# Kernel optimization log

Hardware: AMD Instinct MI355X
Metric: run time of the kernel (lower is better)

Reference implementation:

```python
import jax, jax.numpy as jnp
import numpy as np

D_MODEL = 2816
N_HEADS = 16
DH = 512
N_KV = 2
MAX_CTX = 8192
POS = 4095  # current decode position (0-indexed)
EPS = 1e-6
Q_DIM = N_HEADS * DH
KV_DIM = N_KV * DH
NEG_INF = -1e9


def setup_inputs() -> dict:
    key = jax.random.key(0)
    ks = jax.random.split(key, 8)
    x = jax.random.normal(ks[0], (1, 1, D_MODEL), jnp.float32)
    # Realistic RoPE angles at position POS (full head_dim rotation, half/half layout)
    inv_freq = 1.0 / (10000.0 ** (np.arange(0, DH, 2, dtype=np.float32) / DH))  # (DH/2,)
    ang = POS * inv_freq
    cos = jnp.asarray(np.concatenate([np.cos(ang), np.cos(ang)])[None, None, :], jnp.float32)  # (1,1,DH)
    sin = jnp.asarray(np.concatenate([np.sin(ang), np.sin(ang)])[None, None, :], jnp.float32)
    k_cache = jax.random.normal(ks[1], (1, N_KV, MAX_CTX, DH), jnp.float32) * 0.02
    v_cache = jax.random.normal(ks[2], (1, N_KV, MAX_CTX, DH), jnp.float32) * 0.02
    # causal decode mask: attend to [0, POS], -inf beyond
    pos_ids = jnp.arange(MAX_CTX)
    attn_mask = jnp.where(pos_ids <= POS, 0.0, NEG_INF).astype(jnp.float32).reshape(1, 1, 1, MAX_CTX)
    # one-hot write mask at current position
    kv_write_mask = jnp.zeros((1, 1, MAX_CTX, 1), jnp.float32).at[0, 0, POS, 0].set(1.0)
    Wq = jax.random.normal(ks[3], (Q_DIM, D_MODEL), jnp.float32) * 0.02
    Wk = jax.random.normal(ks[4], (KV_DIM, D_MODEL), jnp.float32) * 0.02
    Wo = jax.random.normal(ks[5], (D_MODEL, Q_DIM), jnp.float32) * 0.02
    q_gamma = jax.random.normal(ks[6], (DH,), jnp.float32) * 0.02  # stored as (gamma-1)
    k_gamma = jax.random.normal(ks[7], (DH,), jnp.float32) * 0.02
    return {"x": x, "cos": cos, "sin": sin, "k_cache": k_cache, "v_cache": v_cache,
            "attn_mask": attn_mask, "kv_write_mask": kv_write_mask,
            "Wq": Wq, "Wk": Wk, "Wo": Wo, "q_gamma": q_gamma, "k_gamma": k_gamma}


def _rmsnorm(x, w=None):
    v = jnp.mean(x * x, axis=-1, keepdims=True)
    x = x * jax.lax.rsqrt(v + EPS)
    return x if w is None else x * (1.0 + w)


def _rope(x, cos, sin):
    # x: (1,T,H,D); cos/sin: (1,T,D)
    c = cos[:, :, None, :]
    s = sin[:, :, None, :]
    d = x.shape[-1]
    x1, x2 = x[..., : d // 2], x[..., d // 2 :]
    rot = jnp.concatenate([-x2, x1], axis=-1)
    return x * c + rot * s


def reference(x, cos, sin, k_cache, v_cache, attn_mask, kv_write_mask, Wq, Wk, Wo, q_gamma, k_gamma):
    q_raw = (x @ Wq.T).reshape(1, 1, N_HEADS, DH)
    k_raw = (x @ Wk.T).reshape(1, 1, N_KV, DH)
    q = _rope(_rmsnorm(q_raw, q_gamma), cos, sin)
    k = _rope(_rmsnorm(k_raw, k_gamma), cos, sin)
    v = _rmsnorm(k_raw)  # unscaled norm, not rotated
    q = jnp.swapaxes(q, 1, 2)  # (1,H,1,D)
    k = jnp.swapaxes(k, 1, 2)  # (1,n_kv,1,D)
    v = jnp.swapaxes(v, 1, 2)
    k_new = k_cache + k * kv_write_mask  # broadcast write at current slot
    v_new = v_cache + v * kv_write_mask
    rep = N_HEADS // N_KV
    K = jnp.repeat(k_new, rep, axis=1)  # (1,H,S,D)
    V = jnp.repeat(v_new, rep, axis=1)
    scores = jnp.einsum("bhtd,bhsd->bhts", q, K) + attn_mask  # no 1/sqrt(d) scale, as in source
    w = jax.nn.softmax(scores.astype(jnp.float32), axis=-1).astype(q.dtype)
    ctx = jnp.einsum("bhts,bhsd->bhtd", w, V)  # (1,H,1,D)
    ctx = jnp.swapaxes(ctx, 1, 2).reshape(1, 1, Q_DIM)
    out = ctx @ Wo.T
    return (out, k_new, v_new)
```

## Files before the change

### kernel.cpp

```cpp
#include <hip/hip_runtime.h>
#include <math.h>

#define D_MODEL 2816
#define N_HEADS 16
#define DH      512
#define N_KV    2
#define MAX_CTX 8192
#define POS     4095
#define EPS     1e-6f
#define Q_DIM   8192
#define KV_DIM  1024
#define GROUP   8
#define NPOS    4096
#define AB      128


__device__ __forceinline__ float4 f4_mul(float4 a, float s) {
  return make_float4(a.x*s, a.y*s, a.z*s, a.w*s);
}
__device__ __forceinline__ float4 f4_mul4(float4 a, float4 b) {
  return make_float4(a.x*b.x, a.y*b.y, a.z*b.z, a.w*b.w);
}
__device__ __forceinline__ float4 f4_fma(float4 a, float4 b, float4 c) {
  return make_float4(fmaf(a.x,b.x,c.x), fmaf(a.y,b.y,c.y), fmaf(a.z,b.z,c.z), fmaf(a.w,b.w,c.w));
}
__device__ __forceinline__ float4 f4_fmas(float s, float4 b, float4 c) {
  return make_float4(fmaf(s,b.x,c.x), fmaf(s,b.y,c.y), fmaf(s,b.z,c.z), fmaf(s,b.w,c.w));
}
__device__ __forceinline__ float4 f4_fnma(float4 a, float4 b, float4 c) {
  return make_float4(fmaf(-a.x,b.x,c.x), fmaf(-a.y,b.y,c.y), fmaf(-a.z,b.z,c.z), fmaf(-a.w,b.w,c.w));
}
__device__ __forceinline__ float4 f4_add(float4 a, float4 b) {
  return make_float4(a.x+b.x, a.y+b.y, a.z+b.z, a.w+b.w);
}
__device__ __forceinline__ float f4_dot(float4 a, float4 b) {
  return a.x*b.x + a.y*b.y + a.z*b.z + a.w*b.w;
}
__device__ __forceinline__ float f4_ssq(float4 a) {
  return a.x*a.x + a.y*a.y + a.z*a.z + a.w*a.w;
}

__global__ __launch_bounds__(256) void k_qkv(const float* __restrict__ x,
    const float* __restrict__ Wq, const float* __restrict__ Wk,
    float* __restrict__ qraw, float* __restrict__ kraw,
    float* __restrict__ ctx, float* __restrict__ lvec) {
  int t = threadIdx.x;
  if (blockIdx.x == 0) {
    float4* c4 = (float4*)ctx;
#pragma unroll
    for (int j = 0; j < 8; ++j) c4[j * 256 + t] = make_float4(0.f, 0.f, 0.f, 0.f);
    if (t < 16) lvec[t] = 0.f;
  }
  int wid  = (blockIdx.x * blockDim.x + t) >> 6;
  int lane = t & 63;
  const float4* x4 = (const float4*)x;
  int row = wid;
  const float4* W4 = (row < Q_DIM)
      ? (const float4*)(Wq + (size_t)row * D_MODEL)
      : (const float4*)(Wk + (size_t)(row - Q_DIM) * D_MODEL);
  float a0 = 0.f, a1 = 0.f;
#pragma unroll
  for (int it = 0; it < D_MODEL / 256; ++it) {
    float d = f4_dot(W4[it * 64 + lane], x4[it * 64 + lane]);
    if (it & 1) a1 += d; else a0 += d;
  }
  float acc = a0 + a1;
#pragma unroll
  for (int m = 32; m; m >>= 1) acc += __shfl_xor(acc, m, 64);
  if (lane == 0) {
    if (row < Q_DIM) qraw[row] = acc;
    else             kraw[row - Q_DIM] = acc;
  }
}

__global__ __launch_bounds__(512) void k_fused(
    const float* __restrict__ kc, const float* __restrict__ vc,
    const float* __restrict__ qraw, const float* __restrict__ kraw,
    const float* __restrict__ cosv, const float* __restrict__ sinv,
    const float* __restrict__ qg,   const float* __restrict__ kg,
    float* __restrict__ knew, float* __restrict__ vnew,
    float* __restrict__ ctx, float* __restrict__ lvec) {
  __shared__ float4 lq[GROUP * 128];
  __shared__ float  pvbuf[8 * 512];
  __shared__ float  lbuf[64];
  __shared__ float4 kfin[128];
  __shared__ float4 vfin[128];
  int b = blockIdx.x;
  int g = b >> 8;
  int rb = b & 255;
  int t = threadIdx.x;
  int w = t >> 6, lane = t & 63;
  bool att = (rb < AB);

  if (att) {
    const float4* c4 = (const float4*)cosv;
    const float4* s4 = (const float4*)sinv;
    float4 c1 = c4[lane],      s1 = s4[lane];
    float4 c2 = c4[64 + lane], s2 = s4[64 + lane];
    const float4* qr4 = (const float4*)(qraw + (size_t)(g * GROUP + w) * DH);
    float4 a  = qr4[lane];
    float4 b2 = qr4[64 + lane];
    float ss = f4_ssq(a) + f4_ssq(b2);
#pragma unroll
    for (int m = 32; m; m >>= 1) ss += __shfl_xor(ss, m, 64);
    float scale = rsqrtf(ss * (1.f / (float)DH) + EPS);
    const float4* qg4 = (const float4*)qg;
    float4 ga = qg4[lane], gb = qg4[64 + lane];
    float4 na = f4_mul4(f4_mul(a,  scale), make_float4(1.f+ga.x,1.f+ga.y,1.f+ga.z,1.f+ga.w));
    float4 nb = f4_mul4(f4_mul(b2, scale), make_float4(1.f+gb.x,1.f+gb.y,1.f+gb.z,1.f+gb.w));
    lq[w * 128 + lane]      = f4_fnma(nb, s1, f4_mul4(na, c1));
    lq[w * 128 + 64 + lane] = f4_fma (na, s2, f4_mul4(nb, c2));
    if (rb == (POS >> 5) && w == 0) {
      const float4* kr4 = (const float4*)(kraw + (size_t)g * DH);
      float4 ka_ = kr4[lane];
      float4 kb_ = kr4[64 + lane];
      float ss2 = f4_ssq(ka_) + f4_ssq(kb_);
#pragma unroll
      for (int m = 32; m; m >>= 1) ss2 += __shfl_xor(ss2, m, 64);
      float sc2 = rsqrtf(ss2 * (1.f / (float)DH) + EPS);
      float4 va_ = f4_mul(ka_, sc2);
      float4 vb_ = f4_mul(kb_, sc2);
      const float4* kg4 = (const float4*)kg;
      float4 ga2 = kg4[lane], gb2 = kg4[64 + lane];
      float4 na2 = f4_mul4(va_, make_float4(1.f+ga2.x,1.f+ga2.y,1.f+ga2.z,1.f+ga2.w));
      float4 nb2 = f4_mul4(vb_, make_float4(1.f+gb2.x,1.f+gb2.y,1.f+gb2.z,1.f+gb2.w));
      kfin[lane]      = f4_fnma(nb2, s1, f4_mul4(na2, c1));
      kfin[64 + lane] = f4_fma (na2, s2, f4_mul4(nb2, c2));
      vfin[lane]      = va_;
      vfin[64 + lane] = vb_;
    }
    __syncthreads();
  }

  float4 acc[GROUP][2];
#pragma unroll
  for (int h = 0; h < GROUP; ++h) { acc[h][0] = make_float4(0,0,0,0); acc[h][1] = make_float4(0,0,0,0); }
  float lacc[GROUP] = {0.f,0.f,0.f,0.f,0.f,0.f,0.f,0.f};

  for (int r = 0; r < 4; ++r) {
    int s = (rb << 5) + (w << 2) + r;
    size_t row = ((size_t)g * MAX_CTX + s) * DH;
    const float4* kc4 = (const float4*)(kc + row);
    const float4* vc4 = (const float4*)(vc + row);
    float4 ka = kc4[lane], kb = kc4[64 + lane];
    float4 va = vc4[lane], vb = vc4[64 + lane];
    if (s == POS) {
      ka = f4_add(ka, kfin[lane]); kb = f4_add(kb, kfin[64 + lane]);
      va = f4_add(va, vfin[lane]); vb = f4_add(vb, vfin[64 + lane]);
    }
    float4* ko4 = (float4*)(knew + row);
    float4* vo4 = (float4*)(vnew + row);
    ko4[lane] = ka; ko4[64 + lane] = kb;
    vo4[lane] = va; vo4[64 + lane] = vb;
    if (att) {
      float sc[GROUP];
#pragma unroll
      for (int h = 0; h < GROUP; ++h)
        sc[h] = f4_dot(lq[h * 128 + lane], ka) + f4_dot(lq[h * 128 + 64 + lane], kb);
#pragma unroll
      for (int h = 0; h < GROUP; ++h) {
#pragma unroll
        for (int m = 32; m; m >>= 1) sc[h] += __shfl_xor(sc[h], m, 64);
      }
#pragma unroll
      for (int h = 0; h < GROUP; ++h) {
        float e = __expf(fminf(sc[h], 80.f));
        lacc[h] += e;
        acc[h][0] = f4_fmas(e, va, acc[h][0]);
        acc[h][1] = f4_fmas(e, vb, acc[h][1]);
      }
    }
  }

  if (att) {
    float4* pv4 = (float4*)pvbuf;
#pragma unroll
    for (int h = 0; h < GROUP; ++h) {
      __syncthreads();
      pv4[w * 128 + lane]      = acc[h][0];
      pv4[w * 128 + 64 + lane] = acc[h][1];
      __syncthreads();
      float sum = 0.f;
#pragma unroll
      for (int w2 = 0; w2 < 8; ++w2) sum += pvbuf[w2 * 512 + t];
      atomicAdd(&ctx[(size_t)(g * GROUP + h) * DH + t], sum);
    }
    float myl = 0.f;
#pragma unroll
    for (int h = 0; h < GROUP; ++h) myl = (lane == h) ? lacc[h] : myl;
    if (lane < 8) lbuf[w * 8 + lane] = myl;
    __syncthreads();
    if (t < 8) {
      float sl = 0.f;
#pragma unroll
      for (int w2 = 0; w2 < 8; ++w2) sl += lbuf[w2 * 8 + t];
      atomicAdd(&lvec[g * GROUP + t], sl);
    }
  }
}

__global__ __launch_bounds__(256) void k_oproj(const float* __restrict__ ctx,
    const float* __restrict__ lvec, const float* __restrict__ Wo,
    float* __restrict__ out) {
  __shared__ float linv[16];
  int t = threadIdx.x;
  if (t < 16) linv[t] = 1.f / lvec[t];
  __syncthreads();
  int wid  = (blockIdx.x * blockDim.x + t) >> 6;
  int lane = t & 63;
  const float4* c4 = (const float4*)ctx;
  int row = wid;
  const float4* W4 = (const float4*)(Wo + (size_t)row * Q_DIM);
  float a0 = 0.f, a1 = 0.f;
#pragma unroll
  for (int it = 0; it < Q_DIM / 256; ++it) {
    float d = f4_dot(W4[it * 64 + lane], c4[it * 64 + lane]) * linv[it >> 1];
    if (it & 1) a1 += d; else a0 += d;
  }
  float acc = a0 + a1;
#pragma unroll
  for (int m = 32; m; m >>= 1) acc += __shfl_xor(acc, m, 64);
  if (lane == 0) out[row] = acc;
}

extern "C" void kernel_launch(void* const* d_in, const int* in_sizes, int n_in,
                              void* d_out, int out_size, void* d_ws, size_t ws_size,
                              hipStream_t stream) {
  (void)in_sizes; (void)n_in; (void)out_size; (void)ws_size;
  const float* x    = (const float*)d_in[0];
  const float* cosv = (const float*)d_in[1];
  const float* sinv = (const float*)d_in[2];
  const float* kc   = (const float*)d_in[3];
  const float* vc   = (const float*)d_in[4];
  const float* Wq   = (const float*)d_in[7];
  const float* Wk   = (const float*)d_in[8];
  const float* Wo   = (const float*)d_in[9];
  const float* qg   = (const float*)d_in[10];
  const float* kg   = (const float*)d_in[11];

  float* out  = (float*)d_out;
  float* knew = out + D_MODEL;
  float* vnew = knew + (size_t)N_KV * MAX_CTX * DH;

  float* w      = (float*)d_ws;
  float* qraw   = w;
  float* kraw   = w + 8192;
  float* ctx    = w + 9216;
  float* lvec   = w + 17408;

  k_qkv  <<<2304, 256, 0, stream>>>(x, Wq, Wk, qraw, kraw, ctx, lvec);
  k_fused<<<512, 512, 0, stream>>>(kc, vc, qraw, kraw, cosv, sinv, qg, kg,
                                   knew, vnew, ctx, lvec);
  k_oproj<<<704, 256, 0, stream>>>(ctx, lvec, Wo, out);
}
```

Before: 72.24 us.

## Move non-attended KV cache copy into QKV matvec kernel and use nontemporal accesses

The copy of the unattended cache half (positions 4096..8191) moves out of the attention kernel and into the first kernel, which now runs both the Q/K matvec blocks and the copy blocks. The bandwidth-bound copy can then overlap the weight-streaming matvec, and the attention kernel shrinks to only the attended blocks. Matvec blocks now handle two rows per wave, and streaming loads and stores of weights and cache use nontemporal builtins to reduce cache pollution. The risk is contention between the copy and matvec for bandwidth, plus a scheduling imbalance between the two block types.

```diff
diff --git a/kernel.cpp b/kernel.cpp
--- a/kernel.cpp
+++ b/kernel.cpp
@@ -12,8 +12,12 @@
 #define KV_DIM  1024
 #define GROUP   8
 #define NPOS    4096
-#define AB      128
-
+
+#define NB_MV   1152
+#define NB_CP   512
+
+
+typedef float nfloat4 __attribute__((ext_vector_type(4)));
 
 __device__ __forceinline__ float4 f4_mul(float4 a, float s) {
   return make_float4(a.x*s, a.y*s, a.z*s, a.w*s);
@@ -39,41 +43,74 @@
 __device__ __forceinline__ float f4_ssq(float4 a) {
   return a.x*a.x + a.y*a.y + a.z*a.z + a.w*a.w;
 }
-
-__global__ __launch_bounds__(256) void k_qkv(const float* __restrict__ x,
+__device__ __forceinline__ float4 ntl(const float4* p) {
+  nfloat4 v = __builtin_nontemporal_load(reinterpret_cast<const nfloat4*>(p));
+  return make_float4(v.x, v.y, v.z, v.w);
+}
+__device__ __forceinline__ void nts(float4* p, float4 v) {
+  nfloat4 nv; nv.x = v.x; nv.y = v.y; nv.z = v.z; nv.w = v.w;
+  __builtin_nontemporal_store(nv, reinterpret_cast<nfloat4*>(p));
+}
+
+__global__ __launch_bounds__(256) void k_a(const float* __restrict__ x,
     const float* __restrict__ Wq, const float* __restrict__ Wk,
+    const float* __restrict__ kc, const float* __restrict__ vc,
+    float* __restrict__ knew, float* __restrict__ vnew,
     float* __restrict__ qraw, float* __restrict__ kraw,
     float* __restrict__ ctx, float* __restrict__ lvec) {
   int t = threadIdx.x;
-  if (blockIdx.x == 0) {
+  int blk = blockIdx.x;
+  int w = t >> 6, lane = t & 63;
+  if (blk == 0) {
     float4* c4 = (float4*)ctx;
 #pragma unroll
     for (int j = 0; j < 8; ++j) c4[j * 256 + t] = make_float4(0.f, 0.f, 0.f, 0.f);
     if (t < 16) lvec[t] = 0.f;
   }
-  int wid  = (blockIdx.x * blockDim.x + t) >> 6;
-  int lane = t & 63;
-  const float4* x4 = (const float4*)x;
-  int row = wid;
-  const float4* W4 = (row < Q_DIM)
-      ? (const float4*)(Wq + (size_t)row * D_MODEL)
-      : (const float4*)(Wk + (size_t)(row - Q_DIM) * D_MODEL);
-  float a0 = 0.f, a1 = 0.f;
-#pragma unroll
-  for (int it = 0; it < D_MODEL / 256; ++it) {
-    float d = f4_dot(W4[it * 64 + lane], x4[it * 64 + lane]);
-    if (it & 1) a1 += d; else a0 += d;
-  }
-  float acc = a0 + a1;
-#pragma unroll
-  for (int m = 32; m; m >>= 1) acc += __shfl_xor(acc, m, 64);
-  if (lane == 0) {
-    if (row < Q_DIM) qraw[row] = acc;
-    else             kraw[row - Q_DIM] = acc;
-  }
-}
-
-__global__ __launch_bounds__(512) void k_fused(
+  if (blk < NB_MV) {
+    const float4* x4 = (const float4*)x;
+    int W = blk * 4 + w;
+#pragma unroll
+    for (int i = 0; i < 2; ++i) {
+      int row = W + i * 4608;
+      const float4* W4 = (row < Q_DIM)
+          ? (const float4*)(Wq + (size_t)row * D_MODEL)
+          : (const float4*)(Wk + (size_t)(row - Q_DIM) * D_MODEL);
+      float a0 = 0.f, a1 = 0.f;
+#pragma unroll
+      for (int it = 0; it < D_MODEL / 256; ++it) {
+        float d = f4_dot(ntl(&W4[it * 64 + lane]), x4[it * 64 + lane]);
+        if (it & 1) a1 += d; else a0 += d;
+      }
+      float acc = a0 + a1;
+#pragma unroll
+      for (int m = 32; m; m >>= 1) acc += __shfl_xor(acc, m, 64);
+      if (lane == 0) {
+        if (row < Q_DIM) qraw[row] = acc;
+        else             kraw[row - Q_DIM] = acc;
+      }
+    }
+  } else {
+    int idx = blk - NB_MV;
+#pragma unroll
+    for (int r = 0; r < 4; ++r) {
+      int u = idx * 16 + w * 4 + r;
+      int g = u >> 12;
+      int s = 4096 + (u & 4095);
+      size_t row = ((size_t)g * MAX_CTX + s) * DH;
+      const float4* kc4 = (const float4*)(kc + row);
+      const float4* vc4 = (const float4*)(vc + row);
+      float4* ko4 = (float4*)(knew + row);
+      float4* vo4 = (float4*)(vnew + row);
+      nts(&ko4[lane],      ntl(&kc4[lane]));
+      nts(&ko4[64 + lane], ntl(&kc4[64 + lane]));
+      nts(&vo4[lane],      ntl(&vc4[lane]));
+      nts(&vo4[64 + lane], ntl(&vc4[64 + lane]));
+    }
+  }
+}
+
+__global__ __launch_bounds__(512) void k_att(
     const float* __restrict__ kc, const float* __restrict__ vc,
     const float* __restrict__ qraw, const float* __restrict__ kraw,
     const float* __restrict__ cosv, const float* __restrict__ sinv,
@@ -86,13 +123,12 @@
   __shared__ float4 kfin[128];
   __shared__ float4 vfin[128];
   int b = blockIdx.x;
-  int g = b >> 8;
-  int rb = b & 255;
+  int g = b >> 7;
+  int rb = b & 127;
   int t = threadIdx.x;
   int w = t >> 6, lane = t & 63;
-  bool att = (rb < AB);
-
-  if (att) {
+
+  {
     const float4* c4 = (const float4*)cosv;
     const float4* s4 = (const float4*)sinv;
     float4 c1 = c4[lane],      s1 = s4[lane];
@@ -142,37 +178,35 @@
     size_t row = ((size_t)g * MAX_CTX + s) * DH;
     const float4* kc4 = (const float4*)(kc + row);
     const float4* vc4 = (const float4*)(vc + row);
-    float4 ka = kc4[lane], kb = kc4[64 + lane];
-    float4 va = vc4[lane], vb = vc4[64 + lane];
+    float4 ka = ntl(&kc4[lane]), kb = ntl(&kc4[64 + lane]);
+    float4 va = ntl(&vc4[lane]), vb = ntl(&vc4[64 + lane]);
     if (s == POS) {
       ka = f4_add(ka, kfin[lane]); kb = f4_add(kb, kfin[64 + lane]);
       va = f4_add(va, vfin[lane]); vb = f4_add(vb, vfin[64 + lane]);
     }
     float4* ko4 = (float4*)(knew + row);
     float4* vo4 = (float4*)(vnew + row);
-    ko4[lane] = ka; ko4[64 + lane] = kb;
-    vo4[lane] = va; vo4[64 + lane] = vb;
-    if (att) {
-      float sc[GROUP];
-#pragma unroll
-      for (int h = 0; h < GROUP; ++h)
-        sc[h] = f4_dot(lq[h * 128 + lane], ka) + f4_dot(lq[h * 128 + 64 + lane], kb);
-#pragma unroll
-      for (int h = 0; h < GROUP; ++h) {
-#pragma unroll
-        for (int m = 32; m; m >>= 1) sc[h] += __shfl_xor(sc[h], m, 64);
-      }
-#pragma unroll
-      for (int h = 0; h < GROUP; ++h) {
-        float e = __expf(fminf(sc[h], 80.f));
-        lacc[h] += e;
-        acc[h][0] = f4_fmas(e, va, acc[h][0]);
-        acc[h][1] = f4_fmas(e, vb, acc[h][1]);
-      }
-    }
-  }
-
-  if (att) {
+    nts(&ko4[lane], ka); nts(&ko4[64 + lane], kb);
+    nts(&vo4[lane], va); nts(&vo4[64 + lane], vb);
+    float sc[GROUP];
+#pragma unroll
+    for (int h = 0; h < GROUP; ++h)
+      sc[h] = f4_dot(lq[h * 128 + lane], ka) + f4_dot(lq[h * 128 + 64 + lane], kb);
+#pragma unroll
+    for (int h = 0; h < GROUP; ++h) {
+#pragma unroll
+      for (int m = 32; m; m >>= 1) sc[h] += __shfl_xor(sc[h], m, 64);
+    }
+#pragma unroll
+    for (int h = 0; h < GROUP; ++h) {
+      float e = __expf(fminf(sc[h], 80.f));
+      lacc[h] += e;
+      acc[h][0] = f4_fmas(e, va, acc[h][0]);
+      acc[h][1] = f4_fmas(e, vb, acc[h][1]);
+    }
+  }
+
+  {
     float4* pv4 = (float4*)pvbuf;
 #pragma unroll
     for (int h = 0; h < GROUP; ++h) {
@@ -214,7 +248,7 @@
   float a0 = 0.f, a1 = 0.f;
 #pragma unroll
   for (int it = 0; it < Q_DIM / 256; ++it) {
-    float d = f4_dot(W4[it * 64 + lane], c4[it * 64 + lane]) * linv[it >> 1];
+    float d = f4_dot(ntl(&W4[it * 64 + lane]), c4[it * 64 + lane]) * linv[it >> 1];
     if (it & 1) a1 += d; else a0 += d;
   }
   float acc = a0 + a1;
@@ -248,8 +282,9 @@
   float* ctx    = w + 9216;
   float* lvec   = w + 17408;
 
-  k_qkv  <<<2304, 256, 0, stream>>>(x, Wq, Wk, qraw, kraw, ctx, lvec);
-  k_fused<<<512, 512, 0, stream>>>(kc, vc, qraw, kraw, cosv, sinv, qg, kg,
+  k_a    <<<NB_MV + NB_CP, 256, 0, stream>>>(x, Wq, Wk, kc, vc, knew, vnew,
+                                             qraw, kraw, ctx, lvec);
+  k_att  <<<256, 512, 0, stream>>>(kc, vc, qraw, kraw, cosv, sinv, qg, kg,
                                    knew, vnew, ctx, lvec);
   k_oproj<<<704, 256, 0, stream>>>(ctx, lvec, Wo, out);
 }
```

Result: faster. 70.43 us (-2.5%).
